# Optimization experiments

Measured on AMD Instinct MI355X. Metric: run time of the kernel, lower is better.

## Reference

```python
import jax, jax.numpy as jnp
import numpy as np

D_MODEL = 1024
NUM_HEADS = 16
KEY_DIM = 64
VALUE_DIM = 64
NEG_INF = jnp.float32(-1e30)


def setup_inputs() -> dict:
    key = jax.random.key(0)
    ks = jax.random.split(key, 10)
    B, S = 2, 2048
    lim = 1.0 / np.sqrt(D_MODEL)
    x = jax.random.normal(ks[0], (B, S, D_MODEL), dtype=jnp.float32)
    mask = jnp.ones((B, S), dtype=jnp.int32)  # pad mask: 1 = keep
    # stacked per-head linear params (Linear stores weight as [out, in])
    Wq = jax.random.uniform(ks[1], (NUM_HEADS, KEY_DIM, D_MODEL), jnp.float32, -lim, lim)
    bq = jax.random.uniform(ks[2], (NUM_HEADS, KEY_DIM), jnp.float32, -lim, lim)
    Wk = jax.random.uniform(ks[3], (NUM_HEADS, KEY_DIM, D_MODEL), jnp.float32, -lim, lim)
    bk = jax.random.uniform(ks[4], (NUM_HEADS, KEY_DIM), jnp.float32, -lim, lim)
    Wv = jax.random.uniform(ks[5], (NUM_HEADS, VALUE_DIM, D_MODEL), jnp.float32, -lim, lim)
    bv = jax.random.uniform(ks[6], (NUM_HEADS, VALUE_DIM), jnp.float32, -lim, lim)
    lim_o = 1.0 / np.sqrt(NUM_HEADS * VALUE_DIM)
    Wo = jax.random.uniform(ks[7], (D_MODEL, NUM_HEADS * VALUE_DIM), jnp.float32, -lim_o, lim_o)
    bo = jax.random.uniform(ks[8], (D_MODEL,), jnp.float32, -lim_o, lim_o)
    return {"x": x, "mask": mask, "Wq": Wq, "bq": bq, "Wk": Wk, "bk": bk,
            "Wv": Wv, "bv": bv, "Wo": Wo, "bo": bo}


def _mha(x, mask, Wq, bq, Wk, bk, Wv, bv, Wo, bo):
    B, S, _ = x.shape
    # per-head projections: [B, H, S, k]
    q = jnp.einsum('bsd,hkd->bhsk', x, Wq) + bq[None, :, None, :]
    k = jnp.einsum('bsd,hkd->bhsk', x, Wk) + bk[None, :, None, :]
    v = jnp.einsum('bsd,hvd->bhsv', x, Wv) + bv[None, :, None, :]
    scale = 1.0 / np.sqrt(KEY_DIM).astype(np.float32)
    scores = jnp.einsum('bhik,bhjk->bhij', q, k) * scale  # [B, H, S, S]
    # final mask = causal AND pad-row AND pad-col
    causal = jnp.tril(jnp.ones((S, S), dtype=bool))
    pad = mask.astype(bool)
    final = causal[None, None] & pad[:, None, :, None] & pad[:, None, None, :]
    masked = jnp.where(final, scores, NEG_INF)
    w = jax.nn.softmax(masked, axis=-1)
    w = jnp.where(final, w, 0.0)  # fully-masked rows -> zeros, matching loop impl
    out = jnp.einsum('bhij,bhjv->bhiv', w, v)            # [B, H, S, V]
    concat = out.transpose(0, 2, 1, 3).reshape(B, S, NUM_HEADS * VALUE_DIM)
    return concat @ Wo.T + bo


def reference(x, mask, Wq, bq, Wk, bk, Wv, bv, Wo, bo):
    return _mha(x, mask, Wq, bq, Wk, bk, Wv, bv, Wo, bo)
```

## Files before the change

### kernel.cpp

```cpp
#include <hip/hip_runtime.h>

#define SEQ 2048
#define NH 16
#define HD 64
#define DMODEL 1024

__device__ __forceinline__ unsigned int f2bf(float f) {
  unsigned int u = __float_as_uint(f);
  return ((u + 0x7fffu + ((u >> 16) & 1u)) >> 16) & 0xffffu;
}

typedef __bf16 bf16x8 __attribute__((ext_vector_type(8)));
typedef float f32x4 __attribute__((ext_vector_type(4)));

__device__ __forceinline__ void gl2lds16(const unsigned short* g, unsigned short* l) {
  __builtin_amdgcn_global_load_lds(
      (const __attribute__((address_space(1))) unsigned int*)g,
      (__attribute__((address_space(3))) unsigned int*)l, 16, 0, 0);
}

__global__ __launch_bounds__(256) void cast_all_kernel(
    const float* __restrict__ x, const float* __restrict__ wq,
    const float* __restrict__ wk, const float* __restrict__ wv,
    const float* __restrict__ wo,
    unsigned short* __restrict__ xb, unsigned short* __restrict__ wqb,
    unsigned short* __restrict__ wkb, unsigned short* __restrict__ wvb,
    unsigned short* __restrict__ wob) {
  int idx = blockIdx.x * 256 + threadIdx.x;
  if (idx >= 1048576) return;
  const float* src;
  unsigned short* dst;
  int off;
  if (idx < 524288) {
    src = x; dst = xb; off = idx;
  } else {
    int t = idx - 524288;
    int w = t >> 17;
    off = t & 131071;
    src = (w == 0) ? wq : (w == 1) ? wk : (w == 2) ? wv : wo;
    dst = (w == 0) ? wqb : (w == 1) ? wkb : (w == 2) ? wvb : wob;
  }
  const float4* p = reinterpret_cast<const float4*>(src) + (size_t)off * 2;
  float4 a = p[0], b = p[1];
  uint4 o;
  o.x = f2bf(a.x) | (f2bf(a.y) << 16);
  o.y = f2bf(a.z) | (f2bf(a.w) << 16);
  o.z = f2bf(b.x) | (f2bf(b.y) << 16);
  o.w = f2bf(b.z) | (f2bf(b.w) << 16);
  reinterpret_cast<uint4*>(dst)[off] = o;
}

template <int MODE>
__global__ __launch_bounds__(256) void gemm128(
    const unsigned short* __restrict__ A, const unsigned short* __restrict__ B,
    const float* __restrict__ bias0, const float* __restrict__ bias1,
    const float* __restrict__ bias2, float* __restrict__ Cf,
    unsigned short* __restrict__ Qo, unsigned short* __restrict__ Ko,
    unsigned short* __restrict__ Vto, int Kdim) {
  __shared__ __align__(16) unsigned short As[128 * 64];
  __shared__ __align__(16) unsigned short Bs[128 * 64];
  const int tid = threadIdx.x;
  const int wave = tid >> 6, lane = tid & 63;
  const int wm = wave >> 1, wn = wave & 1;
  const int fr = lane & 15, quad = lane >> 4;
  const int n0 = blockIdx.x * 128, m0 = blockIdx.y * 128;

  const unsigned short* Abase =
      A + (size_t)(m0 + wave * 32 + (lane >> 3)) * Kdim + (lane & 7) * 8;
  const unsigned short* Bbase =
      B + (size_t)(n0 + wave * 32 + (lane >> 3)) * Kdim + (lane & 7) * 8;
  unsigned short* AsW = As + (wave * 32) * 64;
  unsigned short* BsW = Bs + (wave * 32) * 64;

  f32x4 acc[4][4];
#pragma unroll
  for (int mt = 0; mt < 4; ++mt)
#pragma unroll
    for (int nt = 0; nt < 4; ++nt) acc[mt][nt] = f32x4{0.f, 0.f, 0.f, 0.f};

  for (int k0 = 0; k0 < Kdim; k0 += 64) {
#pragma unroll
    for (int t = 0; t < 4; ++t) {
      gl2lds16(Abase + (size_t)(t * 8) * Kdim + k0, AsW + t * 8 * 64);
      gl2lds16(Bbase + (size_t)(t * 8) * Kdim + k0, BsW + t * 8 * 64);
    }
    __syncthreads();
#pragma unroll
    for (int ks = 0; ks < 2; ++ks) {
      bf16x8 af[4], bfv[4];
#pragma unroll
      for (int mt = 0; mt < 4; ++mt)
        af[mt] = *reinterpret_cast<const bf16x8*>(
            As + (wm * 64 + mt * 16 + fr) * 64 + ks * 32 + quad * 8);
#pragma unroll
      for (int nt = 0; nt < 4; ++nt)
        bfv[nt] = *reinterpret_cast<const bf16x8*>(
            Bs + (wn * 64 + nt * 16 + fr) * 64 + ks * 32 + quad * 8);
#pragma unroll
      for (int mt = 0; mt < 4; ++mt)
#pragma unroll
        for (int nt = 0; nt < 4; ++nt)
          acc[mt][nt] = __builtin_amdgcn_mfma_f32_16x16x32_bf16(
              af[mt], bfv[nt], acc[mt][nt], 0, 0, 0);
    }
    __syncthreads();
  }

  if (MODE == 0) {
    const int seg = n0 >> 10;
    const float* bp = (seg == 0) ? bias0 : (seg == 1) ? bias1 : bias2;
    const float scale = (seg == 0) ? 0.125f : 1.0f;
    unsigned short* QK = (seg == 0) ? Qo : Ko;
#pragma unroll
    for (int nt = 0; nt < 4; ++nt) {
      const int c = (n0 + wn * 64 + nt * 16 + fr) & 1023;
      const int h = c >> 6, d = c & 63;
      const float bs = bp[c];
#pragma unroll
      for (int mt = 0; mt < 4; ++mt) {
        const int mbase = m0 + wm * 64 + mt * 16 + quad * 4;
        const int b = mbase >> 11, s0 = mbase & 2047;
        if (seg < 2) {
          unsigned short* dst = QK + (((size_t)(b * NH + h)) * SEQ + s0) * HD + d;
#pragma unroll
          for (int r = 0; r < 4; ++r)
            dst[(size_t)r * HD] = (unsigned short)f2bf((acc[mt][nt][r] + bs) * scale);
        } else {
          ushort4 pk;
          pk.x = (unsigned short)f2bf(acc[mt][nt][0] + bs);
          pk.y = (unsigned short)f2bf(acc[mt][nt][1] + bs);
          pk.z = (unsigned short)f2bf(acc[mt][nt][2] + bs);
          pk.w = (unsigned short)f2bf(acc[mt][nt][3] + bs);
          *reinterpret_cast<ushort4*>(
              Vto + (((size_t)(b * NH + h)) * HD + d) * SEQ + s0) = pk;
        }
      }
    }
  } else {
#pragma unroll
    for (int nt = 0; nt < 4; ++nt) {
      const int cg = n0 + wn * 64 + nt * 16 + fr;
      const float bs = bias0[cg];
#pragma unroll
      for (int mt = 0; mt < 4; ++mt) {
        const int mbase = m0 + wm * 64 + mt * 16 + quad * 4;
#pragma unroll
        for (int r = 0; r < 4; ++r)
          Cf[(size_t)(mbase + r) * DMODEL + cg] = acc[mt][nt][r] + bs;
      }
    }
  }
}

__global__ __launch_bounds__(256) void attn_mfma_kernel(const unsigned short* __restrict__ Qg,
                                                        const unsigned short* __restrict__ Kg,
                                                        const unsigned short* __restrict__ Vtg,
                                                        const int* __restrict__ mask,
                                                        unsigned short* __restrict__ concat) {
  const int iblock = 31 - (blockIdx.x >> 5);
  const int bh = blockIdx.x & 31;
  const int b = bh >> 4;
  const int h = bh & 15;
  const int tid = threadIdx.x;
  const int wave = tid >> 6;
  const int lane = tid & 63;
  const int quad = lane >> 4;
  const int fr = lane & 15;
  const int i0 = iblock * 64;
  const int irow = i0 + wave * 16 + fr;

  __shared__ unsigned short Ks[64][72];
  __shared__ unsigned short Vts[64][72];
  __shared__ unsigned short Pt[4][16][72];

  const unsigned short* Qb = Qg + ((size_t)bh * SEQ) * HD;
  const unsigned short* Kb = Kg + ((size_t)bh * SEQ) * HD;
  const unsigned short* Vtb = Vtg + ((size_t)bh * HD) * SEQ;
  const int* maskb = mask + b * SEQ;

  const bf16x8 qf0 = *reinterpret_cast<const bf16x8*>(Qb + (size_t)irow * HD + quad * 8);
  const bf16x8 qf1 = *reinterpret_cast<const bf16x8*>(Qb + (size_t)irow * HD + quad * 8 + 32);
  const int padi = maskb[irow];

  f32x4 o[4];
#pragma unroll
  for (int vt = 0; vt < 4; ++vt) o[vt] = f32x4{0.f, 0.f, 0.f, 0.f};
  float mrun = -1e30f, lrun = 0.f;

  const int srow = tid >> 2;
  const int spart = (tid & 3) * 2;

  for (int jc = 0; jc <= iblock; ++jc) {
    const int j0 = jc * 64;
    {
      const uint4* kg = reinterpret_cast<const uint4*>(Kb + (size_t)(j0 + srow) * HD);
      const uint4* vg = reinterpret_cast<const uint4*>(Vtb + (size_t)srow * SEQ + j0);
      uint4 ka = kg[spart], kc = kg[spart + 1];
      uint4 va = vg[spart], vc = vg[spart + 1];
      *reinterpret_cast<uint4*>(&Ks[srow][spart * 8]) = ka;
      *reinterpret_cast<uint4*>(&Ks[srow][spart * 8 + 8]) = kc;
      *reinterpret_cast<uint4*>(&Vts[srow][spart * 8]) = va;
      *reinterpret_cast<uint4*>(&Vts[srow][spart * 8 + 8]) = vc;
    }
    __syncthreads();

    f32x4 st[4];
#pragma unroll
    for (int jt = 0; jt < 4; ++jt) {
      st[jt] = f32x4{0.f, 0.f, 0.f, 0.f};
      bf16x8 ka0 = *reinterpret_cast<const bf16x8*>(&Ks[jt * 16 + fr][quad * 8]);
      bf16x8 ka1 = *reinterpret_cast<const bf16x8*>(&Ks[jt * 16 + fr][quad * 8 + 32]);
      st[jt] = __builtin_amdgcn_mfma_f32_16x16x32_bf16(ka0, qf0, st[jt], 0, 0, 0);
      st[jt] = __builtin_amdgcn_mfma_f32_16x16x32_bf16(ka1, qf1, st[jt], 0, 0, 0);
    }

    const bool diag = (jc == iblock);
    const int4* mp = reinterpret_cast<const int4*>(maskb + j0);
#pragma unroll
    for (int jt = 0; jt < 4; ++jt) {
      const int4 mv = mp[jt * 4 + quad];
      const int jb = j0 + jt * 16 + quad * 4;
      if (mv.x == 0 || (diag && jb + 0 > irow)) st[jt][0] = -1e30f;
      if (mv.y == 0 || (diag && jb + 1 > irow)) st[jt][1] = -1e30f;
      if (mv.z == 0 || (diag && jb + 2 > irow)) st[jt][2] = -1e30f;
      if (mv.w == 0 || (diag && jb + 3 > irow)) st[jt][3] = -1e30f;
    }

    float tmax = -1e30f;
#pragma unroll
    for (int jt = 0; jt < 4; ++jt)
#pragma unroll
      for (int r = 0; r < 4; ++r) tmax = fmaxf(tmax, st[jt][r]);
    tmax = fmaxf(tmax, __shfl_xor(tmax, 16));
    tmax = fmaxf(tmax, __shfl_xor(tmax, 32));
    float mnew = fmaxf(fmaxf(mrun, tmax), -1e20f);
    const float corr = __expf(mrun - mnew);
    float p[16];
    float lloc = 0.f;
#pragma unroll
    for (int jt = 0; jt < 4; ++jt)
#pragma unroll
      for (int r = 0; r < 4; ++r) {
        float pv = __expf(st[jt][r] - mnew);
        p[jt * 4 + r] = pv;
        lloc += pv;
      }
    lloc += __shfl_xor(lloc, 16);
    lloc += __shfl_xor(lloc, 32);
    lrun = lrun * corr + lloc;
    mrun = mnew;

#pragma unroll
    for (int jt = 0; jt < 4; ++jt) {
      ushort4 pk;
      pk.x = (unsigned short)f2bf(p[jt * 4 + 0]);
      pk.y = (unsigned short)f2bf(p[jt * 4 + 1]);
      pk.z = (unsigned short)f2bf(p[jt * 4 + 2]);
      pk.w = (unsigned short)f2bf(p[jt * 4 + 3]);
      *reinterpret_cast<ushort4*>(&Pt[wave][fr][jt * 16 + quad * 4]) = pk;
    }

#pragma unroll
    for (int vt = 0; vt < 4; ++vt) {
      o[vt][0] *= corr; o[vt][1] *= corr; o[vt][2] *= corr; o[vt][3] *= corr;
    }

    bf16x8 pa0 = *reinterpret_cast<const bf16x8*>(&Pt[wave][fr][quad * 8]);
    bf16x8 pa1 = *reinterpret_cast<const bf16x8*>(&Pt[wave][fr][quad * 8 + 32]);
#pragma unroll
    for (int vt = 0; vt < 4; ++vt) {
      bf16x8 vb0 = *reinterpret_cast<const bf16x8*>(&Vts[vt * 16 + fr][quad * 8]);
      bf16x8 vb1 = *reinterpret_cast<const bf16x8*>(&Vts[vt * 16 + fr][quad * 8 + 32]);
      o[vt] = __builtin_amdgcn_mfma_f32_16x16x32_bf16(vb0, pa0, o[vt], 0, 0, 0);
      o[vt] = __builtin_amdgcn_mfma_f32_16x16x32_bf16(vb1, pa1, o[vt], 0, 0, 0);
    }
    __syncthreads();
  }

  const float inv = (padi != 0 && lrun > 0.f) ? 1.f / lrun : 0.f;
  unsigned short* orow = concat + ((size_t)(b * SEQ + irow)) * DMODEL + h * HD;
#pragma unroll
  for (int vt = 0; vt < 4; ++vt) {
    ushort4 pk;
    pk.x = (unsigned short)f2bf(o[vt][0] * inv);
    pk.y = (unsigned short)f2bf(o[vt][1] * inv);
    pk.z = (unsigned short)f2bf(o[vt][2] * inv);
    pk.w = (unsigned short)f2bf(o[vt][3] * inv);
    *reinterpret_cast<ushort4*>(orow + vt * 16 + quad * 4) = pk;
  }
}

extern "C" void kernel_launch(void* const* d_in, const int* in_sizes, int n_in,
                              void* d_out, int out_size, void* d_ws, size_t ws_size,
                              hipStream_t stream) {
  (void)in_sizes; (void)n_in; (void)out_size;
  const float* x  = (const float*)d_in[0];
  const int* mask = (const int*)d_in[1];
  const float* Wq = (const float*)d_in[2];
  const float* bq = (const float*)d_in[3];
  const float* Wk = (const float*)d_in[4];
  const float* bk = (const float*)d_in[5];
  const float* Wv = (const float*)d_in[6];
  const float* bv = (const float*)d_in[7];
  const float* Wo = (const float*)d_in[8];
  const float* bo = (const float*)d_in[9];
  float* out = (float*)d_out;

  char* ws = (char*)d_ws;
  if (ws_size < (48ull << 20)) return;
  unsigned short* xb  = (unsigned short*)(ws);
  unsigned short* wqb = (unsigned short*)(ws + (8ull  << 20));
  unsigned short* wkb = (unsigned short*)(ws + (10ull << 20));
  unsigned short* wvb = (unsigned short*)(ws + (12ull << 20));
  unsigned short* wob = (unsigned short*)(ws + (14ull << 20));
  unsigned short* Qb  = (unsigned short*)(ws + (16ull << 20));
  unsigned short* Kb  = (unsigned short*)(ws + (24ull << 20));
  unsigned short* Vtb = (unsigned short*)(ws + (32ull << 20));
  unsigned short* cb  = (unsigned short*)(ws + (40ull << 20));

  cast_all_kernel<<<4096, 256, 0, stream>>>(x, Wq, Wk, Wv, Wo, xb, wqb, wkb, wvb, wob);

  gemm128<0><<<dim3(24, 32), 256, 0, stream>>>(xb, wqb, bq, bk, bv,
                                               nullptr, Qb, Kb, Vtb, 1024);

  attn_mfma_kernel<<<1024, 256, 0, stream>>>(Qb, Kb, Vtb, mask, cb);

  gemm128<1><<<dim3(8, 32), 256, 0, stream>>>(cb, wob, bo, nullptr, nullptr,
                                              out, nullptr, nullptr, nullptr, 1024);
}
```

Before: 219.8 us.

## Swizzle GEMM LDS layout and process two query tiles per attention block

The GEMM kernel now XOR-swizzles the 16-byte chunk index when staging A/B tiles into LDS and when reading fragments, to avoid LDS bank conflicts on the MFMA fragment loads. The attention kernel now handles 128 query rows per block as two 64-row sub-tiles that share each loaded K/V tile, halving K/V global traffic and staging per query row. The grid is halved to 512 blocks with a reordered block-to-tile mapping meant to balance causal work. The cost is more accumulator registers per thread (two sets of O, m, l), which can lower occupancy, and fewer blocks to spread across CUs.

```diff
diff --git a/kernel.cpp b/kernel.cpp
--- a/kernel.cpp
+++ b/kernel.cpp
@@ -63,12 +63,15 @@
   const int wave = tid >> 6, lane = tid & 63;
   const int wm = wave >> 1, wn = wave & 1;
   const int fr = lane & 15, quad = lane >> 4;
+  const int fx = fr & 7;
   const int n0 = blockIdx.x * 128, m0 = blockIdx.y * 128;
 
+  const int srowg = lane >> 3;
+  const int schunk = (lane & 7) ^ (srowg & 7);
   const unsigned short* Abase =
-      A + (size_t)(m0 + wave * 32 + (lane >> 3)) * Kdim + (lane & 7) * 8;
+      A + (size_t)(m0 + wave * 32 + srowg) * Kdim + schunk * 8;
   const unsigned short* Bbase =
-      B + (size_t)(n0 + wave * 32 + (lane >> 3)) * Kdim + (lane & 7) * 8;
+      B + (size_t)(n0 + wave * 32 + srowg) * Kdim + schunk * 8;
   unsigned short* AsW = As + (wave * 32) * 64;
   unsigned short* BsW = Bs + (wave * 32) * 64;
 
@@ -91,11 +94,11 @@
 #pragma unroll
       for (int mt = 0; mt < 4; ++mt)
         af[mt] = *reinterpret_cast<const bf16x8*>(
-            As + (wm * 64 + mt * 16 + fr) * 64 + ks * 32 + quad * 8);
+            As + (wm * 64 + mt * 16 + fr) * 64 + ((ks * 4 + quad) ^ fx) * 8);
 #pragma unroll
       for (int nt = 0; nt < 4; ++nt)
         bfv[nt] = *reinterpret_cast<const bf16x8*>(
-            Bs + (wn * 64 + nt * 16 + fr) * 64 + ks * 32 + quad * 8);
+            Bs + (wn * 64 + nt * 16 + fr) * 64 + ((ks * 4 + quad) ^ fx) * 8);
 #pragma unroll
       for (int mt = 0; mt < 4; ++mt)
 #pragma unroll
@@ -157,7 +160,8 @@
                                                         const unsigned short* __restrict__ Vtg,
                                                         const int* __restrict__ mask,
                                                         unsigned short* __restrict__ concat) {
-  const int iblock = 31 - (blockIdx.x >> 5);
+  const int group = blockIdx.x >> 5;
+  const int ib = (group < 8) ? (15 - group) : (group - 8);
   const int bh = blockIdx.x & 31;
   const int b = bh >> 4;
   const int h = bh & 15;
@@ -166,8 +170,7 @@
   const int lane = tid & 63;
   const int quad = lane >> 4;
   const int fr = lane & 15;
-  const int i0 = iblock * 64;
-  const int irow = i0 + wave * 16 + fr;
+  const int i0 = ib * 128;
 
   __shared__ unsigned short Ks[64][72];
   __shared__ unsigned short Vts[64][72];
@@ -178,19 +181,29 @@
   const unsigned short* Vtb = Vtg + ((size_t)bh * HD) * SEQ;
   const int* maskb = mask + b * SEQ;
 
-  const bf16x8 qf0 = *reinterpret_cast<const bf16x8*>(Qb + (size_t)irow * HD + quad * 8);
-  const bf16x8 qf1 = *reinterpret_cast<const bf16x8*>(Qb + (size_t)irow * HD + quad * 8 + 32);
-  const int padi = maskb[irow];
-
-  f32x4 o[4];
-#pragma unroll
-  for (int vt = 0; vt < 4; ++vt) o[vt] = f32x4{0.f, 0.f, 0.f, 0.f};
-  float mrun = -1e30f, lrun = 0.f;
+  int irow[2];
+  bf16x8 qf[2][2];
+  int padi[2];
+#pragma unroll
+  for (int qc = 0; qc < 2; ++qc) {
+    irow[qc] = i0 + qc * 64 + wave * 16 + fr;
+    qf[qc][0] = *reinterpret_cast<const bf16x8*>(Qb + (size_t)irow[qc] * HD + quad * 8);
+    qf[qc][1] = *reinterpret_cast<const bf16x8*>(Qb + (size_t)irow[qc] * HD + quad * 8 + 32);
+    padi[qc] = maskb[irow[qc]];
+  }
+
+  f32x4 o[2][4];
+#pragma unroll
+  for (int qc = 0; qc < 2; ++qc)
+#pragma unroll
+    for (int vt = 0; vt < 4; ++vt) o[qc][vt] = f32x4{0.f, 0.f, 0.f, 0.f};
+  float mrun[2] = {-1e30f, -1e30f}, lrun[2] = {0.f, 0.f};
 
   const int srow = tid >> 2;
   const int spart = (tid & 3) * 2;
-
-  for (int jc = 0; jc <= iblock; ++jc) {
+  const int njc = 2 * ib + 2;
+
+  for (int jc = 0; jc < njc; ++jc) {
     const int j0 = jc * 64;
     {
       const uint4* kg = reinterpret_cast<const uint4*>(Kb + (size_t)(j0 + srow) * HD);
@@ -204,89 +217,103 @@
     }
     __syncthreads();
 
-    f32x4 st[4];
-#pragma unroll
-    for (int jt = 0; jt < 4; ++jt) {
-      st[jt] = f32x4{0.f, 0.f, 0.f, 0.f};
-      bf16x8 ka0 = *reinterpret_cast<const bf16x8*>(&Ks[jt * 16 + fr][quad * 8]);
-      bf16x8 ka1 = *reinterpret_cast<const bf16x8*>(&Ks[jt * 16 + fr][quad * 8 + 32]);
-      st[jt] = __builtin_amdgcn_mfma_f32_16x16x32_bf16(ka0, qf0, st[jt], 0, 0, 0);
-      st[jt] = __builtin_amdgcn_mfma_f32_16x16x32_bf16(ka1, qf1, st[jt], 0, 0, 0);
-    }
-
-    const bool diag = (jc == iblock);
     const int4* mp = reinterpret_cast<const int4*>(maskb + j0);
-#pragma unroll
-    for (int jt = 0; jt < 4; ++jt) {
-      const int4 mv = mp[jt * 4 + quad];
-      const int jb = j0 + jt * 16 + quad * 4;
-      if (mv.x == 0 || (diag && jb + 0 > irow)) st[jt][0] = -1e30f;
-      if (mv.y == 0 || (diag && jb + 1 > irow)) st[jt][1] = -1e30f;
-      if (mv.z == 0 || (diag && jb + 2 > irow)) st[jt][2] = -1e30f;
-      if (mv.w == 0 || (diag && jb + 3 > irow)) st[jt][3] = -1e30f;
-    }
-
-    float tmax = -1e30f;
-#pragma unroll
-    for (int jt = 0; jt < 4; ++jt)
-#pragma unroll
-      for (int r = 0; r < 4; ++r) tmax = fmaxf(tmax, st[jt][r]);
-    tmax = fmaxf(tmax, __shfl_xor(tmax, 16));
-    tmax = fmaxf(tmax, __shfl_xor(tmax, 32));
-    float mnew = fmaxf(fmaxf(mrun, tmax), -1e20f);
-    const float corr = __expf(mrun - mnew);
-    float p[16];
-    float lloc = 0.f;
-#pragma unroll
-    for (int jt = 0; jt < 4; ++jt)
-#pragma unroll
-      for (int r = 0; r < 4; ++r) {
-        float pv = __expf(st[jt][r] - mnew);
-        p[jt * 4 + r] = pv;
-        lloc += pv;
-      }
-    lloc += __shfl_xor(lloc, 16);
-    lloc += __shfl_xor(lloc, 32);
-    lrun = lrun * corr + lloc;
-    mrun = mnew;
-
-#pragma unroll
-    for (int jt = 0; jt < 4; ++jt) {
+    int4 mvv[4];
+#pragma unroll
+    for (int jt = 0; jt < 4; ++jt) mvv[jt] = mp[jt * 4 + quad];
+
+#pragma unroll
+    for (int qc = 0; qc < 2; ++qc) {
+      if (qc == 0 && jc == 2 * ib + 1) continue;
+      const bool diag = (jc == 2 * ib + qc);
+      const int ir = irow[qc];
+
+      f32x4 st[4];
+#pragma unroll
+      for (int jt = 0; jt < 4; ++jt) {
+        st[jt] = f32x4{0.f, 0.f, 0.f, 0.f};
+        bf16x8 ka0 = *reinterpret_cast<const bf16x8*>(&Ks[jt * 16 + fr][quad * 8]);
+        bf16x8 ka1 = *reinterpret_cast<const bf16x8*>(&Ks[jt * 16 + fr][quad * 8 + 32]);
+        st[jt] = __builtin_amdgcn_mfma_f32_16x16x32_bf16(ka0, qf[qc][0], st[jt], 0, 0, 0);
+        st[jt] = __builtin_amdgcn_mfma_f32_16x16x32_bf16(ka1, qf[qc][1], st[jt], 0, 0, 0);
+      }
+
+#pragma unroll
+      for (int jt = 0; jt < 4; ++jt) {
+        const int4 mv = mvv[jt];
+        const int jb = j0 + jt * 16 + quad * 4;
+        if (mv.x == 0 || (diag && jb + 0 > ir)) st[jt][0] = -1e30f;
+        if (mv.y == 0 || (diag && jb + 1 > ir)) st[jt][1] = -1e30f;
+        if (mv.z == 0 || (diag && jb + 2 > ir)) st[jt][2] = -1e30f;
+        if (mv.w == 0 || (diag && jb + 3 > ir)) st[jt][3] = -1e30f;
+      }
+
+      float tmax = -1e30f;
+#pragma unroll
+      for (int jt = 0; jt < 4; ++jt)
+#pragma unroll
+        for (int r = 0; r < 4; ++r) tmax = fmaxf(tmax, st[jt][r]);
+      tmax = fmaxf(tmax, __shfl_xor(tmax, 16));
+      tmax = fmaxf(tmax, __shfl_xor(tmax, 32));
+      float mnew = fmaxf(fmaxf(mrun[qc], tmax), -1e20f);
+      const float corr = __expf(mrun[qc] - mnew);
+      float p[16];
+      float lloc = 0.f;
+#pragma unroll
+      for (int jt = 0; jt < 4; ++jt)
+#pragma unroll
+        for (int r = 0; r < 4; ++r) {
+          float pv = __expf(st[jt][r] - mnew);
+          p[jt * 4 + r] = pv;
+          lloc += pv;
+        }
+      lloc += __shfl_xor(lloc, 16);
+      lloc += __shfl_xor(lloc, 32);
+      lrun[qc] = lrun[qc] * corr + lloc;
+      mrun[qc] = mnew;
+
+#pragma unroll
+      for (int jt = 0; jt < 4; ++jt) {
+        ushort4 pk;
+        pk.x = (unsigned short)f2bf(p[jt * 4 + 0]);
+        pk.y = (unsigned short)f2bf(p[jt * 4 + 1]);
+        pk.z = (unsigned short)f2bf(p[jt * 4 + 2]);
+        pk.w = (unsigned short)f2bf(p[jt * 4 + 3]);
+        *reinterpret_cast<ushort4*>(&Pt[wave][fr][jt * 16 + quad * 4]) = pk;
+      }
+
+#pragma unroll
+      for (int vt = 0; vt < 4; ++vt) {
+        o[qc][vt][0] *= corr; o[qc][vt][1] *= corr;
+        o[qc][vt][2] *= corr; o[qc][vt][3] *= corr;
+      }
+
+      bf16x8 pa0 = *reinterpret_cast<const bf16x8*>(&Pt[wave][fr][quad * 8]);
+      bf16x8 pa1 = *reinterpret_cast<const bf16x8*>(&Pt[wave][fr][quad * 8 + 32]);
+#pragma unroll
+      for (int vt = 0; vt < 4; ++vt) {
+        bf16x8 vb0 = *reinterpret_cast<const bf16x8*>(&Vts[vt * 16 + fr][quad * 8]);
+        bf16x8 vb1 = *reinterpret_cast<const bf16x8*>(&Vts[vt * 16 + fr][quad * 8 + 32]);
+        o[qc][vt] = __builtin_amdgcn_mfma_f32_16x16x32_bf16(vb0, pa0, o[qc][vt], 0, 0, 0);
+        o[qc][vt] = __builtin_amdgcn_mfma_f32_16x16x32_bf16(vb1, pa1, o[qc][vt], 0, 0, 0);
+      }
+    }
+    __syncthreads();
+  }
+
+#pragma unroll
+  for (int qc = 0; qc < 2; ++qc) {
+    const float inv = (padi[qc] != 0 && lrun[qc] > 0.f) ? 1.f / lrun[qc] : 0.f;
+    unsigned short* orow = concat + ((size_t)(b * SEQ + irow[qc])) * DMODEL + h * HD;
+#pragma unroll
+    for (int vt = 0; vt < 4; ++vt) {
       ushort4 pk;
-      pk.x = (unsigned short)f2bf(p[jt * 4 + 0]);
-      pk.y = (unsigned short)f2bf(p[jt * 4 + 1]);
-      pk.z = (unsigned short)f2bf(p[jt * 4 + 2]);
-      pk.w = (unsigned short)f2bf(p[jt * 4 + 3]);
-      *reinterpret_cast<ushort4*>(&Pt[wave][fr][jt * 16 + quad * 4]) = pk;
-    }
-
-#pragma unroll
-    for (int vt = 0; vt < 4; ++vt) {
-      o[vt][0] *= corr; o[vt][1] *= corr; o[vt][2] *= corr; o[vt][3] *= corr;
-    }
-
-    bf16x8 pa0 = *reinterpret_cast<const bf16x8*>(&Pt[wave][fr][quad * 8]);
-    bf16x8 pa1 = *reinterpret_cast<const bf16x8*>(&Pt[wave][fr][quad * 8 + 32]);
-#pragma unroll
-    for (int vt = 0; vt < 4; ++vt) {
-      bf16x8 vb0 = *reinterpret_cast<const bf16x8*>(&Vts[vt * 16 + fr][quad * 8]);
-      bf16x8 vb1 = *reinterpret_cast<const bf16x8*>(&Vts[vt * 16 + fr][quad * 8 + 32]);
-      o[vt] = __builtin_amdgcn_mfma_f32_16x16x32_bf16(vb0, pa0, o[vt], 0, 0, 0);
-      o[vt] = __builtin_amdgcn_mfma_f32_16x16x32_bf16(vb1, pa1, o[vt], 0, 0, 0);
-    }
-    __syncthreads();
-  }
-
-  const float inv = (padi != 0 && lrun > 0.f) ? 1.f / lrun : 0.f;
-  unsigned short* orow = concat + ((size_t)(b * SEQ + irow)) * DMODEL + h * HD;
-#pragma unroll
-  for (int vt = 0; vt < 4; ++vt) {
-    ushort4 pk;
-    pk.x = (unsigned short)f2bf(o[vt][0] * inv);
-    pk.y = (unsigned short)f2bf(o[vt][1] * inv);
-    pk.z = (unsigned short)f2bf(o[vt][2] * inv);
-    pk.w = (unsigned short)f2bf(o[vt][3] * inv);
-    *reinterpret_cast<ushort4*>(orow + vt * 16 + quad * 4) = pk;
+      pk.x = (unsigned short)f2bf(o[qc][vt][0] * inv);
+      pk.y = (unsigned short)f2bf(o[qc][vt][1] * inv);
+      pk.z = (unsigned short)f2bf(o[qc][vt][2] * inv);
+      pk.w = (unsigned short)f2bf(o[qc][vt][3] * inv);
+      *reinterpret_cast<ushort4*>(orow + vt * 16 + quad * 4) = pk;
+    }
   }
 }
 
@@ -323,7 +350,7 @@
   gemm128<0><<<dim3(24, 32), 256, 0, stream>>>(xb, wqb, bq, bk, bv,
                                                nullptr, Qb, Kb, Vtb, 1024);
 
-  attn_mfma_kernel<<<1024, 256, 0, stream>>>(Qb, Kb, Vtb, mask, cb);
+  attn_mfma_kernel<<<512, 256, 0, stream>>>(Qb, Kb, Vtb, mask, cb);
 
   gemm128<1><<<dim3(8, 32), 256, 0, stream>>>(cb, wob, bo, nullptr, nullptr,
                                               out, nullptr, nullptr, nullptr, 1024);
```

After: 214.6 us. -2.4%, faster.
